# Kernel tuning notes

Measured on AMD Instinct MI355X. Metric: run time of the kernel, lower is better.

The kernel has to match this reference:

```python
import jax, jax.numpy as jnp
import numpy as np

NUM_LANDMARKS = 256
PINV_ITERS = 6


def iterative_inv(K):
    # Newton-Schulz iterative pseudo-inverse (Nystromformer), K: [B, m, m]
    I = jnp.eye(K.shape[-1], dtype=K.dtype)
    V = K.swapaxes(-1, -2) / (jnp.max(jnp.sum(K, axis=-2)) * jnp.max(jnp.sum(K, axis=-1)))
    for _ in range(PINV_ITERS):
        KV = K @ V
        V = 0.25 * V @ (13.0 * I - KV @ (15.0 * I - KV @ (7.0 * I - KV)))
    return V


def nystrom_attention_matrix(q, k, m):
    # q, k: [B, N, d] -> approximate softmax(q k^T / sqrt(d)) of shape [B, N, N]
    B, N, d = q.shape
    scale = 1.0 / jnp.sqrt(jnp.asarray(d, q.dtype))
    L = N // m
    q_l = q.reshape(B, m, L, d).mean(axis=2)  # landmark queries [B, m, d]
    k_l = k.reshape(B, m, L, d).mean(axis=2)  # landmark keys    [B, m, d]
    k1 = jax.nn.softmax(jnp.einsum('bnd,bmd->bnm', q, k_l) * scale, axis=-1)   # [B, N, m]
    k2 = jax.nn.softmax(jnp.einsum('bld,bmd->blm', q_l, k_l) * scale, axis=-1) # [B, m, m]
    k3 = jax.nn.softmax(jnp.einsum('bmd,bnd->bmn', q_l, k) * scale, axis=-1)   # [B, m, N]
    return (k1 @ iterative_inv(k2)) @ k3  # [B, N, N]


def setup_inputs() -> dict:
    key = jax.random.key(0)
    ks = jax.random.split(key, 8)
    B, C, T, W, H = 2, 64, 4, 32, 32
    d = C // 8
    scale = 0.05  # keep q.k scores in a sane softmax range
    return {
        'x': jax.random.normal(ks[0], (B, C, T, W, H), dtype=jnp.float32),
        'wq': jax.random.normal(ks[1], (d, C), dtype=jnp.float32) * scale,
        'bq': jax.random.normal(ks[2], (d,), dtype=jnp.float32) * scale,
        'wk': jax.random.normal(ks[3], (d, C), dtype=jnp.float32) * scale,
        'bk': jax.random.normal(ks[4], (d,), dtype=jnp.float32) * scale,
        'wv': jax.random.normal(ks[5], (C, C), dtype=jnp.float32) * scale,
        'bv': jax.random.normal(ks[6], (C,), dtype=jnp.float32) * scale,
        'gamma': jax.random.normal(ks[7], (1,), dtype=jnp.float32),
    }


def reference(x, wq, bq, wk, bk, wv, bv, gamma):
    B, C, T, W, H = x.shape
    N = T * W * H
    xf = x.reshape(B, C, N)
    # 1x1x1 Conv3d == per-token linear over channels
    q = jnp.einsum('oc,bcn->bno', wq, xf) + bq            # [B, N, C//8]
    k = jnp.einsum('oc,bcn->bno', wk, xf) + bk            # [B, N, C//8]
    v = jnp.einsum('oc,bcn->bon', wv, xf) + bv[None, :, None]  # [B, C, N]
    attn = nystrom_attention_matrix(q, k, NUM_LANDMARKS)  # [B, N, N]
    # out = bmm(value, attn^T): out[b,c,i] = sum_j v[b,c,j] * attn[b,i,j]
    out = jnp.einsum('bcj,bij->bci', v, attn).reshape(B, C, T, W, H)
    out = gamma[0] * out + x
    return out, attn
```

## Files before the change

kernel.cpp:

```cpp
#include <hip/hip_runtime.h>
#include <hip/hip_bf16.h>
#include <math.h>

#define NB 2
#define NC 64
#define ND 8
#define NN 4096
#define NM 256
#define NL 16
#define SCALE 0.35355339059327373f

typedef __attribute__((ext_vector_type(4))) float f32x4;
typedef __attribute__((ext_vector_type(8))) short bf16x8;

__device__ inline ushort f2bf(float f) {
  __hip_bfloat16 h = __float2bfloat16(f);
  return *reinterpret_cast<ushort*>(&h);
}
__device__ inline float bf2f(ushort u) {
  return __uint_as_float(((unsigned int)u) << 16);
}

__device__ inline void gl_lds16(const void* g, void* l) {
  __builtin_amdgcn_global_load_lds(
      (const __attribute__((address_space(1))) unsigned int*)g,
      (__attribute__((address_space(3))) unsigned int*)l, 16, 0, 0);
}

__global__ __launch_bounds__(256) void qkv2_kernel(
    const float* __restrict__ x,
    const float* __restrict__ wq, const float* __restrict__ bq,
    const float* __restrict__ wk, const float* __restrict__ bk,
    const float* __restrict__ wv, const float* __restrict__ bv,
    float* __restrict__ q, float* __restrict__ k, float* __restrict__ v) {
  __shared__ float ws[NC];
  int o = blockIdx.x;
  int b = blockIdx.z;
  int n0 = blockIdx.y * 1024;
  int t = threadIdx.x;
  const float* wrow;
  float bias;
  if (o < ND)            { wrow = wq + (size_t)o * NC;            bias = bq[o]; }
  else if (o < 2 * ND)   { wrow = wk + (size_t)(o - ND) * NC;     bias = bk[o - ND]; }
  else                   { wrow = wv + (size_t)(o - 2 * ND) * NC; bias = bv[o - 2 * ND]; }
  if (t < NC) ws[t] = wrow[t];
  __syncthreads();
  int n = n0 + t * 4;
  float4 acc = {bias, bias, bias, bias};
  #pragma unroll
  for (int c = 0; c < NC; ++c) {
    float wc = ws[c];
    float4 xv = *(const float4*)(x + ((size_t)b * NC + c) * NN + n);
    acc.x += wc * xv.x; acc.y += wc * xv.y; acc.z += wc * xv.z; acc.w += wc * xv.w;
  }
  if (o < ND) {
    float* qp = q + ((size_t)b * NN + n) * ND + o;
    qp[0] = acc.x; qp[8] = acc.y; qp[16] = acc.z; qp[24] = acc.w;
  } else if (o < 2 * ND) {
    float* kp = k + ((size_t)b * NN + n) * ND + (o - ND);
    kp[0] = acc.x; kp[8] = acc.y; kp[16] = acc.z; kp[24] = acc.w;
  } else {
    *(float4*)(v + ((size_t)b * NC + (o - 2 * ND)) * NN + n) = acc;
  }
}

__global__ void landmark_kernel(const float* __restrict__ q, const float* __restrict__ k,
                                float* __restrict__ ql, float* __restrict__ kl) {
  int idx = blockIdx.x * 256 + threadIdx.x;
  int b = idx / (NM * ND), r = idx % (NM * ND), i = r / ND, o = r % ND;
  float sq = 0.f, sk = 0.f;
  for (int l = 0; l < NL; ++l) {
    size_t base = ((size_t)b * NN + i * NL + l) * ND + o;
    sq += q[base]; sk += k[base];
  }
  ql[idx] = sq * (1.0f / NL);
  kl[idx] = sk * (1.0f / NL);
}

__global__ __launch_bounds__(256) void scores_softmax_m_bf16(
    const float* __restrict__ Q, int R, const float* __restrict__ KL,
    ushort* __restrict__ out) {
  __shared__ float skl[NM][9];
  int b = blockIdx.y;
  int t = threadIdx.x;
  for (int i = t; i < NM * ND; i += 256) skl[i >> 3][i & 7] = KL[(size_t)b * NM * ND + i];
  __syncthreads();
  int wave = t >> 6, lane = t & 63;
  int r = blockIdx.x * 4 + wave;
  const float* qrow = Q + ((size_t)b * R + r) * ND;
  float qr[ND];
  #pragma unroll
  for (int dd = 0; dd < ND; ++dd) qr[dd] = qrow[dd];
  float sc[4];
  float lmax = -1e30f;
  #pragma unroll
  for (int s = 0; s < 4; ++s) {
    int j = lane + 64 * s;
    float a = 0.f;
    #pragma unroll
    for (int dd = 0; dd < ND; ++dd) a += qr[dd] * skl[j][dd];
    sc[s] = a * SCALE;
    lmax = fmaxf(lmax, sc[s]);
  }
  for (int off = 32; off; off >>= 1) lmax = fmaxf(lmax, __shfl_xor(lmax, off));
  float lsum = 0.f;
  #pragma unroll
  for (int s = 0; s < 4; ++s) { sc[s] = expf(sc[s] - lmax); lsum += sc[s]; }
  for (int off = 32; off; off >>= 1) lsum += __shfl_xor(lsum, off);
  float inv = 1.0f / lsum;
  #pragma unroll
  for (int s = 0; s < 4; ++s)
    out[((size_t)b * R + r) * NM + lane + 64 * s] = f2bf(sc[s] * inv);
}

__global__ __launch_bounds__(256) void scores_softmax_m_f32(
    const float* __restrict__ Q, int R, const float* __restrict__ KL,
    float* __restrict__ out) {
  __shared__ float skl[NM][9];
  int b = blockIdx.y;
  int t = threadIdx.x;
  for (int i = t; i < NM * ND; i += 256) skl[i >> 3][i & 7] = KL[(size_t)b * NM * ND + i];
  __syncthreads();
  int wave = t >> 6, lane = t & 63;
  int r = blockIdx.x * 4 + wave;
  const float* qrow = Q + ((size_t)b * R + r) * ND;
  float qr[ND];
  #pragma unroll
  for (int dd = 0; dd < ND; ++dd) qr[dd] = qrow[dd];
  float sc[4];
  float lmax = -1e30f;
  #pragma unroll
  for (int s = 0; s < 4; ++s) {
    int j = lane + 64 * s;
    float a = 0.f;
    #pragma unroll
    for (int dd = 0; dd < ND; ++dd) a += qr[dd] * skl[j][dd];
    sc[s] = a * SCALE;
    lmax = fmaxf(lmax, sc[s]);
  }
  for (int off = 32; off; off >>= 1) lmax = fmaxf(lmax, __shfl_xor(lmax, off));
  float lsum = 0.f;
  #pragma unroll
  for (int s = 0; s < 4; ++s) { sc[s] = expf(sc[s] - lmax); lsum += sc[s]; }
  for (int off = 32; off; off >>= 1) lsum += __shfl_xor(lsum, off);
  float inv = 1.0f / lsum;
  #pragma unroll
  for (int s = 0; s < 4; ++s) out[((size_t)b * R + r) * NM + lane + 64 * s] = sc[s] * inv;
}

__global__ __launch_bounds__(256) void scores_softmax_n(
    const float* __restrict__ QL, const float* __restrict__ Kt,
    float* __restrict__ out) {
  __shared__ float wred[4], wsum[4];
  int b = blockIdx.y, i = blockIdx.x;
  int t = threadIdx.x;
  float qr[ND];
  #pragma unroll
  for (int dd = 0; dd < ND; ++dd) qr[dd] = QL[((size_t)b * NM + i) * ND + dd];
  float sc[16];
  float lmax = -1e30f;
  #pragma unroll
  for (int s = 0; s < 16; ++s) {
    int n = t + 256 * s;
    const float* kp = Kt + ((size_t)b * NN + n) * ND;
    float a = 0.f;
    #pragma unroll
    for (int dd = 0; dd < ND; ++dd) a += qr[dd] * kp[dd];
    sc[s] = a * SCALE;
    lmax = fmaxf(lmax, sc[s]);
  }
  for (int off = 32; off; off >>= 1) lmax = fmaxf(lmax, __shfl_xor(lmax, off));
  if ((t & 63) == 0) wred[t >> 6] = lmax;
  __syncthreads();
  lmax = fmaxf(fmaxf(wred[0], wred[1]), fmaxf(wred[2], wred[3]));
  float lsum = 0.f;
  #pragma unroll
  for (int s = 0; s < 16; ++s) { sc[s] = expf(sc[s] - lmax); lsum += sc[s]; }
  for (int off = 32; off; off >>= 1) lsum += __shfl_xor(lsum, off);
  if ((t & 63) == 0) wsum[t >> 6] = lsum;
  __syncthreads();
  lsum = wsum[0] + wsum[1] + wsum[2] + wsum[3];
  float inv = 1.0f / lsum;
  #pragma unroll
  for (int s = 0; s < 16; ++s) out[((size_t)b * NM + i) * NN + t + 256 * s] = sc[s] * inv;
}

__global__ __launch_bounds__(256) void denom_kernel(const float* __restrict__ k2,
                                                    float* __restrict__ denw) {
  __shared__ float red[256];
  int b = blockIdx.x;
  int t = threadIdx.x;
  float cs = 0.f;
  for (int i = 0; i < NM; ++i) cs += k2[((size_t)b * NM + i) * NM + t];
  red[t] = cs;
  __syncthreads();
  for (int off = 128; off; off >>= 1) {
    if (t < off) red[t] = fmaxf(red[t], red[t + off]);
    __syncthreads();
  }
  if (t == 0) denw[b] = red[0];
}

__global__ void vinit_kernel(const float* __restrict__ k2, const float* __restrict__ denw,
                             float* __restrict__ V) {
  int idx = blockIdx.x * 256 + threadIdx.x;
  int b = idx / (NM * NM), r = idx % (NM * NM), i = r / NM, j = r % NM;
  float dval = 1.0f / fmaxf(denw[0], denw[1]);
  V[idx] = k2[((size_t)b * NM + j) * NM + i] * dval;
}

__global__ __launch_bounds__(256) void gemm_rk32(
    const float* __restrict__ A, const float* __restrict__ Bm,
    float* __restrict__ out, float s_a, float s_ab) {
  int b = blockIdx.z;
  int bi = blockIdx.y * 32, bj = blockIdx.x * 32;
  __shared__ float As[32][260];
  __shared__ float Bs[256][36];
  int t = threadIdx.x;
  const float* Ab = A + (size_t)b * NM * NM;
  const float* Bb = Bm + (size_t)b * NM * NM;
  #pragma unroll
  for (int q = 0; q < 8; ++q) {
    int s = q * 256 + t;
    int ar = s >> 6, ac = (s & 63) * 4;
    *(float4*)&As[ar][ac] = *(const float4*)(Ab + (size_t)(bi + ar) * NM + ac);
    int br = s >> 3, bc = (s & 7) * 4;
    *(float4*)&Bs[br][bc] = *(const float4*)(Bb + (size_t)br * NM + bj + bc);
  }
  __syncthreads();
  int tx = t & 15, ty = t >> 4;
  float acc[2][2] = {};
  #pragma unroll 8
  for (int kk = 0; kk < NM; ++kk) {
    float a0 = As[ty * 2][kk], a1 = As[ty * 2 + 1][kk];
    float b0 = Bs[kk][tx * 2], b1 = Bs[kk][tx * 2 + 1];
    acc[0][0] += a0 * b0; acc[0][1] += a0 * b1;
    acc[1][0] += a1 * b0; acc[1][1] += a1 * b1;
  }
  #pragma unroll
  for (int i = 0; i < 2; ++i)
    #pragma unroll
    for (int j = 0; j < 2; ++j) {
      size_t o = ((size_t)b * NM + bi + ty * 2 + i) * NM + bj + tx * 2 + j;
      float r = s_ab * acc[i][j];
      if (s_a != 0.0f) r += s_a * A[o];
      out[o] = r;
    }
}

__global__ __launch_bounds__(256) void cvt_vinv_kernel(const float* __restrict__ Va,
                                                       ushort* __restrict__ Vt) {
  int b = blockIdx.z;
  int n0 = blockIdx.x * 32, m0 = blockIdx.y * 32;
  __shared__ float tile[32][33];
  int t = threadIdx.x;
  int r = t >> 3, c4 = (t & 7) * 4;
  float4 v = *(const float4*)(Va + ((size_t)b * NM + m0 + r) * NM + n0 + c4);
  tile[c4][r] = v.x; tile[c4 + 1][r] = v.y; tile[c4 + 2][r] = v.z; tile[c4 + 3][r] = v.w;
  __syncthreads();
  ushort4 u;
  u.x = f2bf(tile[r][c4]);     u.y = f2bf(tile[r][c4 + 1]);
  u.z = f2bf(tile[r][c4 + 2]); u.w = f2bf(tile[r][c4 + 3]);
  *(ushort4*)(Vt + ((size_t)b * NM + n0 + r) * NM + m0 + c4) = u;
}

__global__ __launch_bounds__(256) void cvt_t_kernel(const float* __restrict__ k3,
                                                    ushort* __restrict__ k3t) {
  int b = blockIdx.z;
  int n0 = blockIdx.x * 32, m0 = blockIdx.y * 32;
  __shared__ float tile[32][33];
  int t = threadIdx.x;
  int r = t >> 3, c4 = (t & 7) * 4;
  float4 v = *(const float4*)(k3 + ((size_t)b * NM + m0 + r) * NN + n0 + c4);
  tile[c4][r] = v.x; tile[c4 + 1][r] = v.y; tile[c4 + 2][r] = v.z; tile[c4 + 3][r] = v.w;
  __syncthreads();
  ushort4 u;
  u.x = f2bf(tile[r][c4]);     u.y = f2bf(tile[r][c4 + 1]);
  u.z = f2bf(tile[r][c4 + 2]); u.w = f2bf(tile[r][c4 + 3]);
  *(ushort4*)(k3t + ((size_t)b * NN + n0 + r) * NM + m0 + c4) = u;
}

__global__ __launch_bounds__(256) void gemm_a_mfma(
    const ushort* __restrict__ k1bf, const ushort* __restrict__ Vt,
    ushort* __restrict__ Abf) {
  int b = blockIdx.z;
  int bi = blockIdx.y * 128, bj = blockIdx.x * 128;
  __shared__ ushort As[128 * 64];
  __shared__ ushort Bs[128 * 64];
  int t = threadIdx.x;
  int wave = t >> 6, lane = t & 63;
  int wr = wave >> 1, wc = wave & 1;
  const ushort* Ab = k1bf + (size_t)b * NN * NM;
  const ushort* Bb = Vt + (size_t)b * NM * NM;
  f32x4 acc[4][4] = {};
  for (int k0 = 0; k0 < NM; k0 += 64) {
    #pragma unroll
    for (int q = 0; q < 4; ++q) {
      int s = q * 256 + t;
      int r = s >> 3, c = s & 7;
      int cs = (c ^ (r & 7)) << 3;
      gl_lds16(Ab + (size_t)(bi + r) * NM + k0 + cs, As + (size_t)s * 8);
      gl_lds16(Bb + (size_t)(bj + r) * NM + k0 + cs, Bs + (size_t)s * 8);
    }
    __syncthreads();
    #pragma unroll
    for (int kk = 0; kk < 2; ++kk) {
      int koff = kk * 64 + (lane >> 4) * 16;
      bf16x8 af[4], bfv[4];
      #pragma unroll
      for (int mi = 0; mi < 4; ++mi) {
        int row = wr * 64 + mi * 16 + (lane & 15);
        af[mi] = *(const bf16x8*)((const char*)As + row * 128 + (koff ^ ((row & 7) << 4)));
      }
      #pragma unroll
      for (int nj = 0; nj < 4; ++nj) {
        int row = wc * 64 + nj * 16 + (lane & 15);
        bfv[nj] = *(const bf16x8*)((const char*)Bs + row * 128 + (koff ^ ((row & 7) << 4)));
      }
      #pragma unroll
      for (int mi = 0; mi < 4; ++mi)
        #pragma unroll
        for (int nj = 0; nj < 4; ++nj)
          acc[mi][nj] = __builtin_amdgcn_mfma_f32_16x16x32_bf16(af[mi], bfv[nj], acc[mi][nj], 0, 0, 0);
    }
    __syncthreads();
  }
  int col = lane & 15, rbase = (lane >> 4) * 4;
  #pragma unroll
  for (int mi = 0; mi < 4; ++mi)
    #pragma unroll
    for (int nj = 0; nj < 4; ++nj)
      #pragma unroll
      for (int r = 0; r < 4; ++r)
        Abf[((size_t)b * NN + bi + wr * 64 + mi * 16 + rbase + r) * NM
            + bj + wc * 64 + nj * 16 + col] = f2bf(acc[mi][nj][r]);
}

__global__ __launch_bounds__(256) void gemm_attn_mfma(
    const ushort* __restrict__ Abf, const ushort* __restrict__ K3T,
    float* __restrict__ attn) {
  int lin = blockIdx.z * 1024 + blockIdx.y * 32 + blockIdx.x;
  int swz = (lin & 7) * 256 + (lin >> 3);
  int b = swz >> 10;
  int rem = swz & 1023;
  int bi = (rem >> 5) * 128, bj = (rem & 31) * 128;
  __shared__ ushort As[128 * 64];
  __shared__ ushort Bs[128 * 64];
  int t = threadIdx.x;
  int wave = t >> 6, lane = t & 63;
  int wr = wave >> 1, wc = wave & 1;
  const ushort* Ab = Abf + (size_t)b * NN * NM;
  const ushort* Bb = K3T + (size_t)b * NN * NM;
  f32x4 acc[4][4] = {};
  for (int k0 = 0; k0 < NM; k0 += 64) {
    #pragma unroll
    for (int q = 0; q < 4; ++q) {
      int s = q * 256 + t;
      int r = s >> 3, c = s & 7;
      int cs = (c ^ (r & 7)) << 3;
      gl_lds16(Ab + (size_t)(bi + r) * NM + k0 + cs, As + (size_t)s * 8);
      gl_lds16(Bb + (size_t)(bj + r) * NM + k0 + cs, Bs + (size_t)s * 8);
    }
    __syncthreads();
    #pragma unroll
    for (int kk = 0; kk < 2; ++kk) {
      int koff = kk * 64 + (lane >> 4) * 16;
      bf16x8 af[4], bfv[4];
      #pragma unroll
      for (int mi = 0; mi < 4; ++mi) {
        int row = wr * 64 + mi * 16 + (lane & 15);
        af[mi] = *(const bf16x8*)((const char*)As + row * 128 + (koff ^ ((row & 7) << 4)));
      }
      #pragma unroll
      for (int nj = 0; nj < 4; ++nj) {
        int row = wc * 64 + nj * 16 + (lane & 15);
        bfv[nj] = *(const bf16x8*)((const char*)Bs + row * 128 + (koff ^ ((row & 7) << 4)));
      }
      #pragma unroll
      for (int mi = 0; mi < 4; ++mi)
        #pragma unroll
        for (int nj = 0; nj < 4; ++nj)
          acc[mi][nj] = __builtin_amdgcn_mfma_f32_16x16x32_bf16(af[mi], bfv[nj], acc[mi][nj], 0, 0, 0);
    }
    __syncthreads();
  }
  int col = lane & 15, rbase = (lane >> 4) * 4;
  #pragma unroll
  for (int mi = 0; mi < 4; ++mi)
    #pragma unroll
    for (int nj = 0; nj < 4; ++nj)
      #pragma unroll
      for (int r = 0; r < 4; ++r)
        attn[((size_t)b * NN + bi + wr * 64 + mi * 16 + rbase + r) * NN
             + bj + wc * 64 + nj * 16 + col] = acc[mi][nj][r];
}

__global__ __launch_bounds__(256) void kv_kernel(
    const float* __restrict__ K3, const float* __restrict__ Vv,
    float* __restrict__ kvout) {
  int b = blockIdx.z, bp = blockIdx.x * 64;
  int j0base = blockIdx.y * (NN / 32);
  __shared__ float Ks[64][33], Vs[64][33];
  int t = threadIdx.x, tx = t & 15, ty = t >> 4;
  int lrow = t >> 2, ljc = (t & 3) * 8;
  float acc[4][4] = {};
  for (int j0 = j0base; j0 < j0base + NN / 32; j0 += 32) {
    float4 a0 = *(const float4*)(K3 + ((size_t)b * NM + bp + lrow) * NN + j0 + ljc);
    float4 a1 = *(const float4*)(K3 + ((size_t)b * NM + bp + lrow) * NN + j0 + ljc + 4);
    float4 v0 = *(const float4*)(Vv + ((size_t)b * NC + lrow) * NN + j0 + ljc);
    float4 v1 = *(const float4*)(Vv + ((size_t)b * NC + lrow) * NN + j0 + ljc + 4);
    Ks[lrow][ljc + 0] = a0.x; Ks[lrow][ljc + 1] = a0.y; Ks[lrow][ljc + 2] = a0.z; Ks[lrow][ljc + 3] = a0.w;
    Ks[lrow][ljc + 4] = a1.x; Ks[lrow][ljc + 5] = a1.y; Ks[lrow][ljc + 6] = a1.z; Ks[lrow][ljc + 7] = a1.w;
    Vs[lrow][ljc + 0] = v0.x; Vs[lrow][ljc + 1] = v0.y; Vs[lrow][ljc + 2] = v0.z; Vs[lrow][ljc + 3] = v0.w;
    Vs[lrow][ljc + 4] = v1.x; Vs[lrow][ljc + 5] = v1.y; Vs[lrow][ljc + 6] = v1.z; Vs[lrow][ljc + 7] = v1.w;
    __syncthreads();
    #pragma unroll
    for (int kk = 0; kk < 32; ++kk) {
      float av_[4], bv_[4];
      #pragma unroll
      for (int i = 0; i < 4; ++i) av_[i] = Ks[(ty << 2) + i][kk];
      #pragma unroll
      for (int j = 0; j < 4; ++j) bv_[j] = Vs[(tx << 2) + j][kk];
      #pragma unroll
      for (int i = 0; i < 4; ++i)
        #pragma unroll
        for (int j = 0; j < 4; ++j) acc[i][j] += av_[i] * bv_[j];
    }
    __syncthreads();
  }
  #pragma unroll
  for (int i = 0; i < 4; ++i)
    #pragma unroll
    for (int j = 0; j < 4; ++j)
      atomicAdd(&kvout[((size_t)b * NM + bp + (ty << 2) + i) * NC + (tx << 2) + j], acc[i][j]);
}

__global__ __launch_bounds__(256) void out_kernel(
    const ushort* __restrict__ Abf, const float* __restrict__ kvm,
    const float* __restrict__ x, const float* __restrict__ gamma,
    float* __restrict__ outp) {
  __shared__ float As[32 * 256];
  int blk = blockIdx.x;
  int b = blk / (NN / 32), n0 = (blk % (NN / 32)) * 32;
  int t = threadIdx.x;
  for (int it = 0; it < 32; ++it)
    As[it * 256 + (t ^ (it & 31))] = bf2f(Abf[((size_t)b * NN + n0 + it) * NM + t]);
  __syncthreads();
  int tn = t & 31, cg0 = (t >> 5) * 8;
  float g = gamma[0];
  float acc[8] = {};
  for (int p = 0; p < NM; ++p) {
    float a = As[tn * 256 + (p ^ (tn & 31))];
    float4 kv0 = *(const float4*)(kvm + ((size_t)b * NM + p) * NC + cg0);
    float4 kv1 = *(const float4*)(kvm + ((size_t)b * NM + p) * NC + cg0 + 4);
    acc[0] += a * kv0.x; acc[1] += a * kv0.y; acc[2] += a * kv0.z; acc[3] += a * kv0.w;
    acc[4] += a * kv1.x; acc[5] += a * kv1.y; acc[6] += a * kv1.z; acc[7] += a * kv1.w;
  }
  #pragma unroll
  for (int qd = 0; qd < 8; ++qd) {
    int c = cg0 + qd;
    size_t idx = ((size_t)b * NC + c) * NN + n0 + tn;
    outp[idx] = g * acc[qd] + x[idx];
  }
}

extern "C" void kernel_launch(void* const* d_in, const int* in_sizes, int n_in,
                              void* d_out, int out_size, void* d_ws, size_t ws_size,
                              hipStream_t stream) {
  const float* x     = (const float*)d_in[0];
  const float* wq    = (const float*)d_in[1];
  const float* bq    = (const float*)d_in[2];
  const float* wk    = (const float*)d_in[3];
  const float* bk    = (const float*)d_in[4];
  const float* wv    = (const float*)d_in[5];
  const float* bv    = (const float*)d_in[6];
  const float* gamma = (const float*)d_in[7];
  float* outp = (float*)d_out;
  float* attn = outp + (size_t)NB * NC * NN;
  float* w = (float*)d_ws;

  float* qw   = w;
  float* kw   = qw + 65536;
  float* vw   = kw + 65536;
  float* qlw  = vw + 524288;
  float* klw  = qlw + 4096;
  float* k1w  = klw + 4096;
  float* k2w  = k1w + 2097152;
  float* k3w  = k2w + 131072;
  float* Abuf = k3w + 2097152;
  float* Va   = Abuf + 2097152;
  float* Vb   = Va + 131072;
  float* Zb   = Vb + 131072;
  float* T1   = Zb + 131072;
  float* T2   = T1 + 131072;
  float* kvw  = T2 + 131072;
  float* denw = kvw + 32768;
  ushort* k1bf  = (ushort*)k1w;
  ushort* k3T   = (ushort*)k1w + 2097152;
  ushort* Abf   = (ushort*)Abuf;
  ushort* Vinvt = (ushort*)Zb;

  hipMemsetAsync(kvw, 0, (size_t)NB * NM * NC * sizeof(float), stream);
  qkv2_kernel<<<dim3(80, NN / 1024, NB), dim3(256), 0, stream>>>(
      x, wq, bq, wk, bk, wv, bv, qw, kw, vw);
  landmark_kernel<<<dim3(NB * NM * ND / 256), dim3(256), 0, stream>>>(qw, kw, qlw, klw);
  scores_softmax_m_bf16<<<dim3(NN / 4, NB), dim3(256), 0, stream>>>(qw, NN, klw, k1bf);
  scores_softmax_m_f32<<<dim3(NM / 4, NB), dim3(256), 0, stream>>>(qlw, NM, klw, k2w);
  scores_softmax_n<<<dim3(NM, NB), dim3(256), 0, stream>>>(qlw, kw, k3w);
  denom_kernel<<<dim3(NB), dim3(256), 0, stream>>>(k2w, denw);
  vinit_kernel<<<dim3(NB * NM * NM / 256), dim3(256), 0, stream>>>(k2w, denw, Va);

  float* Vc = Va; float* Vn = Vb;
  for (int it = 0; it < 6; ++it) {
    gemm_rk32<<<dim3(8, 8, NB), dim3(256), 0, stream>>>(k2w, Vc, Zb, 0.f, 1.f);
    gemm_rk32<<<dim3(8, 8, NB), dim3(256), 0, stream>>>(Zb, Zb, T1, 7.f, -1.f);
    gemm_rk32<<<dim3(8, 8, NB), dim3(256), 0, stream>>>(Zb, T1, T2, 15.f, -1.f);
    gemm_rk32<<<dim3(8, 8, NB), dim3(256), 0, stream>>>(Vc, T2, Vn, 3.25f, -0.25f);
    float* tmp = Vc; Vc = Vn; Vn = tmp;
  }

  cvt_vinv_kernel<<<dim3(NM / 32, NM / 32, NB), dim3(256), 0, stream>>>(Va, Vinvt);
  cvt_t_kernel<<<dim3(NN / 32, NM / 32, NB), dim3(256), 0, stream>>>(k3w, k3T);
  gemm_a_mfma<<<dim3(NM / 128, NN / 128, NB), dim3(256), 0, stream>>>(k1bf, Vinvt, Abf);
  gemm_attn_mfma<<<dim3(NN / 128, NN / 128, NB), dim3(256), 0, stream>>>(Abf, k3T, attn);
  kv_kernel<<<dim3(NM / 64, 32, NB), dim3(256), 0, stream>>>(k3w, vw, kvw);
  out_kernel<<<dim3(NB * NN / 32), dim3(256), 0, stream>>>(Abf, kvw, x, gamma, outp);
}
```

Before: 303.2 us.

## Fuse small kernels and split-K the Newton-Schulz GEMMs with lazy partial sums

The landmark mean is folded into the QKV projection through warp shuffles. The three softmax score kernels and the kv memset are merged into one multi-role launch, and the denominator is merged with the k3 transpose. Attention and kv GEMMs share one launch using a block swizzle. The Newton-Schulz GEMMs become split-K (two K halves written to separate buffers) with 64-thread blocks, and the consumer sums the partial buffers on load. V init is folded in via a transposed, scaled load mode. The aim is to cut launch count and raise parallelism in the small 256x256 iteration GEMMs, at the cost of extra partial-buffer traffic and low occupancy per block.

```diff
diff --git a/kernel.cpp b/kernel.cpp
--- a/kernel.cpp
+++ b/kernel.cpp
@@ -9,6 +9,7 @@
 #define NM 256
 #define NL 16
 #define SCALE 0.35355339059327373f
+#define PS (NB * NM * NM)
 
 typedef __attribute__((ext_vector_type(4))) float f32x4;
 typedef __attribute__((ext_vector_type(8))) short bf16x8;
@@ -27,12 +28,13 @@
       (__attribute__((address_space(3))) unsigned int*)l, 16, 0, 0);
 }
 
-__global__ __launch_bounds__(256) void qkv2_kernel(
+__global__ __launch_bounds__(256) void qkv2l_kernel(
     const float* __restrict__ x,
     const float* __restrict__ wq, const float* __restrict__ bq,
     const float* __restrict__ wk, const float* __restrict__ bk,
     const float* __restrict__ wv, const float* __restrict__ bv,
-    float* __restrict__ q, float* __restrict__ k, float* __restrict__ v) {
+    float* __restrict__ q, float* __restrict__ k, float* __restrict__ v,
+    float* __restrict__ ql, float* __restrict__ kl) {
   __shared__ float ws[NC];
   int o = blockIdx.x;
   int b = blockIdx.z;
@@ -62,222 +64,264 @@
   } else {
     *(float4*)(v + ((size_t)b * NC + (o - 2 * ND)) * NN + n) = acc;
   }
-}
-
-__global__ void landmark_kernel(const float* __restrict__ q, const float* __restrict__ k,
-                                float* __restrict__ ql, float* __restrict__ kl) {
-  int idx = blockIdx.x * 256 + threadIdx.x;
-  int b = idx / (NM * ND), r = idx % (NM * ND), i = r / ND, o = r % ND;
-  float sq = 0.f, sk = 0.f;
-  for (int l = 0; l < NL; ++l) {
-    size_t base = ((size_t)b * NN + i * NL + l) * ND + o;
-    sq += q[base]; sk += k[base];
-  }
-  ql[idx] = sq * (1.0f / NL);
-  kl[idx] = sk * (1.0f / NL);
-}
-
-__global__ __launch_bounds__(256) void scores_softmax_m_bf16(
-    const float* __restrict__ Q, int R, const float* __restrict__ KL,
-    ushort* __restrict__ out) {
+  if (o < 2 * ND) {
+    float s4 = acc.x + acc.y + acc.z + acc.w;
+    s4 += __shfl_xor(s4, 1);
+    s4 += __shfl_xor(s4, 2);
+    if ((t & 3) == 0) {
+      int g = n0 / 16 + (t >> 2);
+      float* dst = (o < ND) ? ql : kl;
+      dst[((size_t)b * NM + g) * ND + (o & 7)] = s4 * (1.0f / 16.0f);
+    }
+  }
+}
+
+__global__ __launch_bounds__(256) void scores_all_kernel(
+    const float* __restrict__ q, const float* __restrict__ ql,
+    const float* __restrict__ kw, const float* __restrict__ kl,
+    ushort* __restrict__ k1bf, float* __restrict__ k2w,
+    float* __restrict__ k3w, float* __restrict__ kvw) {
   __shared__ float skl[NM][9];
-  int b = blockIdx.y;
-  int t = threadIdx.x;
-  for (int i = t; i < NM * ND; i += 256) skl[i >> 3][i & 7] = KL[(size_t)b * NM * ND + i];
+  __shared__ float wred[4], wsum[4];
+  int blk = blockIdx.x;
+  int t = threadIdx.x;
+  if (blk < 2048 + 128) {
+    const float* Q; int R, b, xrow;
+    bool isbf;
+    if (blk < 2048) { b = blk >> 10; xrow = blk & 1023; Q = q;  R = NN; isbf = true; }
+    else { int r = blk - 2048; b = r >> 6; xrow = r & 63; Q = ql; R = NM; isbf = false; }
+    for (int i = t; i < NM * ND; i += 256) skl[i >> 3][i & 7] = kl[(size_t)b * NM * ND + i];
+    __syncthreads();
+    int wave = t >> 6, lane = t & 63;
+    int r = xrow * 4 + wave;
+    const float* qrow = Q + ((size_t)b * R + r) * ND;
+    float qr[ND];
+    #pragma unroll
+    for (int dd = 0; dd < ND; ++dd) qr[dd] = qrow[dd];
+    float sc[4];
+    float lmax = -1e30f;
+    #pragma unroll
+    for (int s = 0; s < 4; ++s) {
+      int j = lane + 64 * s;
+      float a = 0.f;
+      #pragma unroll
+      for (int dd = 0; dd < ND; ++dd) a += qr[dd] * skl[j][dd];
+      sc[s] = a * SCALE;
+      lmax = fmaxf(lmax, sc[s]);
+    }
+    for (int off = 32; off; off >>= 1) lmax = fmaxf(lmax, __shfl_xor(lmax, off));
+    float lsum = 0.f;
+    #pragma unroll
+    for (int s = 0; s < 4; ++s) { sc[s] = expf(sc[s] - lmax); lsum += sc[s]; }
+    for (int off = 32; off; off >>= 1) lsum += __shfl_xor(lsum, off);
+    float inv = 1.0f / lsum;
+    if (isbf) {
+      #pragma unroll
+      for (int s = 0; s < 4; ++s)
+        k1bf[((size_t)b * R + r) * NM + lane + 64 * s] = f2bf(sc[s] * inv);
+    } else {
+      #pragma unroll
+      for (int s = 0; s < 4; ++s)
+        k2w[((size_t)b * R + r) * NM + lane + 64 * s] = sc[s] * inv;
+    }
+  } else if (blk < 2048 + 128 + 512) {
+    int r = blk - 2176;
+    int b = r >> 8, i = r & 255;
+    float qr[ND];
+    #pragma unroll
+    for (int dd = 0; dd < ND; ++dd) qr[dd] = ql[((size_t)b * NM + i) * ND + dd];
+    float sc[16];
+    float lmax = -1e30f;
+    #pragma unroll
+    for (int s = 0; s < 16; ++s) {
+      int n = t + 256 * s;
+      const float* kp = kw + ((size_t)b * NN + n) * ND;
+      float a = 0.f;
+      #pragma unroll
+      for (int dd = 0; dd < ND; ++dd) a += qr[dd] * kp[dd];
+      sc[s] = a * SCALE;
+      lmax = fmaxf(lmax, sc[s]);
+    }
+    for (int off = 32; off; off >>= 1) lmax = fmaxf(lmax, __shfl_xor(lmax, off));
+    if ((t & 63) == 0) wred[t >> 6] = lmax;
+    __syncthreads();
+    lmax = fmaxf(fmaxf(wred[0], wred[1]), fmaxf(wred[2], wred[3]));
+    float lsum = 0.f;
+    #pragma unroll
+    for (int s = 0; s < 16; ++s) { sc[s] = expf(sc[s] - lmax); lsum += sc[s]; }
+    for (int off = 32; off; off >>= 1) lsum += __shfl_xor(lsum, off);
+    if ((t & 63) == 0) wsum[t >> 6] = lsum;
+    __syncthreads();
+    lsum = wsum[0] + wsum[1] + wsum[2] + wsum[3];
+    float inv = 1.0f / lsum;
+    #pragma unroll
+    for (int s = 0; s < 16; ++s) k3w[((size_t)b * NM + i) * NN + t + 256 * s] = sc[s] * inv;
+  } else {
+    int r = blk - 2688;
+    kvw[r * 256 + t] = 0.0f;
+  }
+}
+
+__global__ __launch_bounds__(256) void denom_k3t_kernel(
+    const float* __restrict__ k2, float* __restrict__ denw,
+    const float* __restrict__ k3, ushort* __restrict__ k3t) {
+  __shared__ float red[256];
+  __shared__ float tile[32][33];
+  int blk = blockIdx.x;
+  int t = threadIdx.x;
+  if (blk < NB) {
+    int b = blk;
+    float cs = 0.f;
+    for (int i = 0; i < NM; ++i) cs += k2[((size_t)b * NM + i) * NM + t];
+    red[t] = cs;
+    __syncthreads();
+    for (int off = 128; off; off >>= 1) {
+      if (t < off) red[t] = fmaxf(red[t], red[t + off]);
+      __syncthreads();
+    }
+    if (t == 0) denw[b] = red[0];
+  } else {
+    int r = blk - NB;
+    int n0 = (r & 127) * 32, m0 = ((r >> 7) & 7) * 32, b = r >> 10;
+    int rr = t >> 3, c4 = (t & 7) * 4;
+    float4 v = *(const float4*)(k3 + ((size_t)b * NM + m0 + rr) * NN + n0 + c4);
+    tile[c4][rr] = v.x; tile[c4 + 1][rr] = v.y; tile[c4 + 2][rr] = v.z; tile[c4 + 3][rr] = v.w;
+    __syncthreads();
+    ushort4 u;
+    u.x = f2bf(tile[rr][c4]);     u.y = f2bf(tile[rr][c4 + 1]);
+    u.z = f2bf(tile[rr][c4 + 2]); u.w = f2bf(tile[rr][c4 + 3]);
+    *(ushort4*)(k3t + ((size_t)b * NN + n0 + rr) * NM + m0 + c4) = u;
+  }
+}
+
+__global__ __launch_bounds__(64) void ns_gemm(
+    const float* __restrict__ A, int amode,
+    const float* __restrict__ B, int bmode,
+    const float* __restrict__ denw, float* __restrict__ O,
+    float s_a, float s_ab) {
+  __shared__ float As[128][36];
+  __shared__ float Bs[128][36];
+  int t = threadIdx.x;
+  int bj = blockIdx.x * 32, bi = blockIdx.y * 32;
+  int b = blockIdx.z >> 1, slice = blockIdx.z & 1;
+  int k0 = slice * 128;
+  size_t bo = (size_t)b * NM * NM;
+  float dval = (amode == 2 || bmode == 2) ? 1.0f / fmaxf(denw[0], denw[1]) : 0.f;
+  {
+    int r = t >> 1, kc0 = (t & 1) * 64;
+    if (amode == 2) {
+      for (int i = 0; i < 64; ++i) {
+        int kk = kc0 + i;
+        As[kk][r] = A[bo + (size_t)(k0 + kk) * NM + bi + r] * dval;
+      }
+    } else if (amode == 1) {
+      for (int i = 0; i < 16; ++i) {
+        const float* p = A + bo + (size_t)(bi + r) * NM + k0 + kc0 + i * 4;
+        float4 v0 = *(const float4*)p;
+        float4 v1 = *(const float4*)(p + PS);
+        As[kc0 + i * 4 + 0][r] = v0.x + v1.x;
+        As[kc0 + i * 4 + 1][r] = v0.y + v1.y;
+        As[kc0 + i * 4 + 2][r] = v0.z + v1.z;
+        As[kc0 + i * 4 + 3][r] = v0.w + v1.w;
+      }
+    } else {
+      for (int i = 0; i < 16; ++i) {
+        float4 v0 = *(const float4*)(A + bo + (size_t)(bi + r) * NM + k0 + kc0 + i * 4);
+        As[kc0 + i * 4 + 0][r] = v0.x;
+        As[kc0 + i * 4 + 1][r] = v0.y;
+        As[kc0 + i * 4 + 2][r] = v0.z;
+        As[kc0 + i * 4 + 3][r] = v0.w;
+      }
+    }
+    if (bmode == 2) {
+      for (int i2 = 0; i2 < 2; ++i2) {
+        int kr = t + 64 * i2;
+        for (int c = 0; c < 32; ++c)
+          Bs[kr][c] = B[bo + (size_t)(bj + c) * NM + k0 + kr] * dval;
+      }
+    } else if (bmode == 1) {
+      for (int i2 = 0; i2 < 2; ++i2) {
+        int kr = t + 64 * i2;
+        for (int c4 = 0; c4 < 32; c4 += 4) {
+          const float* p = B + bo + (size_t)(k0 + kr) * NM + bj + c4;
+          float4 v0 = *(const float4*)p;
+          float4 v1 = *(const float4*)(p + PS);
+          v0.x += v1.x; v0.y += v1.y; v0.z += v1.z; v0.w += v1.w;
+          *(float4*)&Bs[kr][c4] = v0;
+        }
+      }
+    } else {
+      for (int i2 = 0; i2 < 2; ++i2) {
+        int kr = t + 64 * i2;
+        for (int c4 = 0; c4 < 32; c4 += 4)
+          *(float4*)&Bs[kr][c4] =
+              *(const float4*)(B + bo + (size_t)(k0 + kr) * NM + bj + c4);
+      }
+    }
+  }
   __syncthreads();
-  int wave = t >> 6, lane = t & 63;
-  int r = blockIdx.x * 4 + wave;
-  const float* qrow = Q + ((size_t)b * R + r) * ND;
-  float qr[ND];
+  int tx = t & 7, ty = t >> 3;
+  float acc[4][4] = {};
+  #pragma unroll 4
+  for (int kk = 0; kk < 128; ++kk) {
+    float4 a4 = *(const float4*)&As[kk][ty * 4];
+    float4 b4 = *(const float4*)&Bs[kk][tx * 4];
+    float av[4] = {a4.x, a4.y, a4.z, a4.w};
+    float bv[4] = {b4.x, b4.y, b4.z, b4.w};
+    #pragma unroll
+    for (int i = 0; i < 4; ++i)
+      #pragma unroll
+      for (int j = 0; j < 4; ++j) acc[i][j] += av[i] * bv[j];
+  }
+  float* Op = O + (size_t)slice * PS + bo;
+  bool addA = (slice == 0) && (s_a != 0.0f);
   #pragma unroll
-  for (int dd = 0; dd < ND; ++dd) qr[dd] = qrow[dd];
-  float sc[4];
-  float lmax = -1e30f;
-  #pragma unroll
-  for (int s = 0; s < 4; ++s) {
-    int j = lane + 64 * s;
-    float a = 0.f;
-    #pragma unroll
-    for (int dd = 0; dd < ND; ++dd) a += qr[dd] * skl[j][dd];
-    sc[s] = a * SCALE;
-    lmax = fmaxf(lmax, sc[s]);
-  }
-  for (int off = 32; off; off >>= 1) lmax = fmaxf(lmax, __shfl_xor(lmax, off));
-  float lsum = 0.f;
-  #pragma unroll
-  for (int s = 0; s < 4; ++s) { sc[s] = expf(sc[s] - lmax); lsum += sc[s]; }
-  for (int off = 32; off; off >>= 1) lsum += __shfl_xor(lsum, off);
-  float inv = 1.0f / lsum;
-  #pragma unroll
-  for (int s = 0; s < 4; ++s)
-    out[((size_t)b * R + r) * NM + lane + 64 * s] = f2bf(sc[s] * inv);
-}
-
-__global__ __launch_bounds__(256) void scores_softmax_m_f32(
-    const float* __restrict__ Q, int R, const float* __restrict__ KL,
-    float* __restrict__ out) {
-  __shared__ float skl[NM][9];
-  int b = blockIdx.y;
-  int t = threadIdx.x;
-  for (int i = t; i < NM * ND; i += 256) skl[i >> 3][i & 7] = KL[(size_t)b * NM * ND + i];
-  __syncthreads();
-  int wave = t >> 6, lane = t & 63;
-  int r = blockIdx.x * 4 + wave;
-  const float* qrow = Q + ((size_t)b * R + r) * ND;
-  float qr[ND];
-  #pragma unroll
-  for (int dd = 0; dd < ND; ++dd) qr[dd] = qrow[dd];
-  float sc[4];
-  float lmax = -1e30f;
-  #pragma unroll
-  for (int s = 0; s < 4; ++s) {
-    int j = lane + 64 * s;
-    float a = 0.f;
-    #pragma unroll
-    for (int dd = 0; dd < ND; ++dd) a += qr[dd] * skl[j][dd];
-    sc[s] = a * SCALE;
-    lmax = fmaxf(lmax, sc[s]);
-  }
-  for (int off = 32; off; off >>= 1) lmax = fmaxf(lmax, __shfl_xor(lmax, off));
-  float lsum = 0.f;
-  #pragma unroll
-  for (int s = 0; s < 4; ++s) { sc[s] = expf(sc[s] - lmax); lsum += sc[s]; }
-  for (int off = 32; off; off >>= 1) lsum += __shfl_xor(lsum, off);
-  float inv = 1.0f / lsum;
-  #pragma unroll
-  for (int s = 0; s < 4; ++s) out[((size_t)b * R + r) * NM + lane + 64 * s] = sc[s] * inv;
-}
-
-__global__ __launch_bounds__(256) void scores_softmax_n(
-    const float* __restrict__ QL, const float* __restrict__ Kt,
-    float* __restrict__ out) {
-  __shared__ float wred[4], wsum[4];
-  int b = blockIdx.y, i = blockIdx.x;
-  int t = threadIdx.x;
-  float qr[ND];
-  #pragma unroll
-  for (int dd = 0; dd < ND; ++dd) qr[dd] = QL[((size_t)b * NM + i) * ND + dd];
-  float sc[16];
-  float lmax = -1e30f;
-  #pragma unroll
-  for (int s = 0; s < 16; ++s) {
-    int n = t + 256 * s;
-    const float* kp = Kt + ((size_t)b * NN + n) * ND;
-    float a = 0.f;
-    #pragma unroll
-    for (int dd = 0; dd < ND; ++dd) a += qr[dd] * kp[dd];
-    sc[s] = a * SCALE;
-    lmax = fmaxf(lmax, sc[s]);
-  }
-  for (int off = 32; off; off >>= 1) lmax = fmaxf(lmax, __shfl_xor(lmax, off));
-  if ((t & 63) == 0) wred[t >> 6] = lmax;
-  __syncthreads();
-  lmax = fmaxf(fmaxf(wred[0], wred[1]), fmaxf(wred[2], wred[3]));
-  float lsum = 0.f;
-  #pragma unroll
-  for (int s = 0; s < 16; ++s) { sc[s] = expf(sc[s] - lmax); lsum += sc[s]; }
-  for (int off = 32; off; off >>= 1) lsum += __shfl_xor(lsum, off);
-  if ((t & 63) == 0) wsum[t >> 6] = lsum;
-  __syncthreads();
-  lsum = wsum[0] + wsum[1] + wsum[2] + wsum[3];
-  float inv = 1.0f / lsum;
-  #pragma unroll
-  for (int s = 0; s < 16; ++s) out[((size_t)b * NM + i) * NN + t + 256 * s] = sc[s] * inv;
-}
-
-__global__ __launch_bounds__(256) void denom_kernel(const float* __restrict__ k2,
-                                                    float* __restrict__ denw) {
-  __shared__ float red[256];
-  int b = blockIdx.x;
-  int t = threadIdx.x;
-  float cs = 0.f;
-  for (int i = 0; i < NM; ++i) cs += k2[((size_t)b * NM + i) * NM + t];
-  red[t] = cs;
-  __syncthreads();
-  for (int off = 128; off; off >>= 1) {
-    if (t < off) red[t] = fmaxf(red[t], red[t + off]);
-    __syncthreads();
-  }
-  if (t == 0) denw[b] = red[0];
-}
-
-__global__ void vinit_kernel(const float* __restrict__ k2, const float* __restrict__ denw,
-                             float* __restrict__ V) {
-  int idx = blockIdx.x * 256 + threadIdx.x;
-  int b = idx / (NM * NM), r = idx % (NM * NM), i = r / NM, j = r % NM;
-  float dval = 1.0f / fmaxf(denw[0], denw[1]);
-  V[idx] = k2[((size_t)b * NM + j) * NM + i] * dval;
-}
-
-__global__ __launch_bounds__(256) void gemm_rk32(
-    const float* __restrict__ A, const float* __restrict__ Bm,
-    float* __restrict__ out, float s_a, float s_ab) {
-  int b = blockIdx.z;
-  int bi = blockIdx.y * 32, bj = blockIdx.x * 32;
-  __shared__ float As[32][260];
-  __shared__ float Bs[256][36];
-  int t = threadIdx.x;
-  const float* Ab = A + (size_t)b * NM * NM;
-  const float* Bb = Bm + (size_t)b * NM * NM;
-  #pragma unroll
-  for (int q = 0; q < 8; ++q) {
-    int s = q * 256 + t;
-    int ar = s >> 6, ac = (s & 63) * 4;
-    *(float4*)&As[ar][ac] = *(const float4*)(Ab + (size_t)(bi + ar) * NM + ac);
-    int br = s >> 3, bc = (s & 7) * 4;
-    *(float4*)&Bs[br][bc] = *(const float4*)(Bb + (size_t)br * NM + bj + bc);
-  }
-  __syncthreads();
-  int tx = t & 15, ty = t >> 4;
-  float acc[2][2] = {};
-  #pragma unroll 8
-  for (int kk = 0; kk < NM; ++kk) {
-    float a0 = As[ty * 2][kk], a1 = As[ty * 2 + 1][kk];
-    float b0 = Bs[kk][tx * 2], b1 = Bs[kk][tx * 2 + 1];
-    acc[0][0] += a0 * b0; acc[0][1] += a0 * b1;
-    acc[1][0] += a1 * b0; acc[1][1] += a1 * b1;
-  }
-  #pragma unroll
-  for (int i = 0; i < 2; ++i)
-    #pragma unroll
-    for (int j = 0; j < 2; ++j) {
-      size_t o = ((size_t)b * NM + bi + ty * 2 + i) * NM + bj + tx * 2 + j;
-      float r = s_ab * acc[i][j];
-      if (s_a != 0.0f) r += s_a * A[o];
-      out[o] = r;
-    }
-}
-
-__global__ __launch_bounds__(256) void cvt_vinv_kernel(const float* __restrict__ Va,
+  for (int i = 0; i < 4; ++i) {
+    int row = bi + ty * 4 + i;
+    float4 rv;
+    rv.x = s_ab * acc[i][0]; rv.y = s_ab * acc[i][1];
+    rv.z = s_ab * acc[i][2]; rv.w = s_ab * acc[i][3];
+    if (addA) {
+      int col = bj + tx * 4;
+      if (amode == 2) {
+        rv.x += s_a * A[bo + (size_t)(col + 0) * NM + row] * dval;
+        rv.y += s_a * A[bo + (size_t)(col + 1) * NM + row] * dval;
+        rv.z += s_a * A[bo + (size_t)(col + 2) * NM + row] * dval;
+        rv.w += s_a * A[bo + (size_t)(col + 3) * NM + row] * dval;
+      } else if (amode == 1) {
+        const float* p = A + bo + (size_t)row * NM + col;
+        float4 a0 = *(const float4*)p;
+        float4 a1 = *(const float4*)(p + PS);
+        rv.x += s_a * (a0.x + a1.x); rv.y += s_a * (a0.y + a1.y);
+        rv.z += s_a * (a0.z + a1.z); rv.w += s_a * (a0.w + a1.w);
+      } else {
+        float4 a0 = *(const float4*)(A + bo + (size_t)row * NM + col);
+        rv.x += s_a * a0.x; rv.y += s_a * a0.y;
+        rv.z += s_a * a0.z; rv.w += s_a * a0.w;
+      }
+    }
+    *(float4*)(Op + (size_t)row * NM + bj + tx * 4) = rv;
+  }
+}
+
+__global__ __launch_bounds__(256) void cvt_vinv_kernel(const float* __restrict__ Vp,
                                                        ushort* __restrict__ Vt) {
   int b = blockIdx.z;
   int n0 = blockIdx.x * 32, m0 = blockIdx.y * 32;
   __shared__ float tile[32][33];
   int t = threadIdx.x;
   int r = t >> 3, c4 = (t & 7) * 4;
-  float4 v = *(const float4*)(Va + ((size_t)b * NM + m0 + r) * NM + n0 + c4);
-  tile[c4][r] = v.x; tile[c4 + 1][r] = v.y; tile[c4 + 2][r] = v.z; tile[c4 + 3][r] = v.w;
+  size_t bo = (size_t)b * NM * NM;
+  const float* p = Vp + bo + (size_t)(m0 + r) * NM + n0 + c4;
+  float4 v0 = *(const float4*)p;
+  float4 v1 = *(const float4*)(p + PS);
+  tile[c4][r] = v0.x + v1.x; tile[c4 + 1][r] = v0.y + v1.y;
+  tile[c4 + 2][r] = v0.z + v1.z; tile[c4 + 3][r] = v0.w + v1.w;
   __syncthreads();
   ushort4 u;
   u.x = f2bf(tile[r][c4]);     u.y = f2bf(tile[r][c4 + 1]);
   u.z = f2bf(tile[r][c4 + 2]); u.w = f2bf(tile[r][c4 + 3]);
-  *(ushort4*)(Vt + ((size_t)b * NM + n0 + r) * NM + m0 + c4) = u;
-}
-
-__global__ __launch_bounds__(256) void cvt_t_kernel(const float* __restrict__ k3,
-                                                    ushort* __restrict__ k3t) {
-  int b = blockIdx.z;
-  int n0 = blockIdx.x * 32, m0 = blockIdx.y * 32;
-  __shared__ float tile[32][33];
-  int t = threadIdx.x;
-  int r = t >> 3, c4 = (t & 7) * 4;
-  float4 v = *(const float4*)(k3 + ((size_t)b * NM + m0 + r) * NN + n0 + c4);
-  tile[c4][r] = v.x; tile[c4 + 1][r] = v.y; tile[c4 + 2][r] = v.z; tile[c4 + 3][r] = v.w;
-  __syncthreads();
-  ushort4 u;
-  u.x = f2bf(tile[r][c4]);     u.y = f2bf(tile[r][c4 + 1]);
-  u.z = f2bf(tile[r][c4 + 2]); u.w = f2bf(tile[r][c4 + 3]);
-  *(ushort4*)(k3t + ((size_t)b * NN + n0 + r) * NM + m0 + c4) = u;
+  *(ushort4*)(Vt + bo + (size_t)(n0 + r) * NM + m0 + c4) = u;
 }
 
 __global__ __launch_bounds__(256) void gemm_a_mfma(
@@ -336,103 +380,108 @@
             + bj + wc * 64 + nj * 16 + col] = f2bf(acc[mi][nj][r]);
 }
 
-__global__ __launch_bounds__(256) void gemm_attn_mfma(
+__global__ __launch_bounds__(256) void attn_kv_kernel(
     const ushort* __restrict__ Abf, const ushort* __restrict__ K3T,
-    float* __restrict__ attn) {
-  int lin = blockIdx.z * 1024 + blockIdx.y * 32 + blockIdx.x;
-  int swz = (lin & 7) * 256 + (lin >> 3);
-  int b = swz >> 10;
-  int rem = swz & 1023;
-  int bi = (rem >> 5) * 128, bj = (rem & 31) * 128;
-  __shared__ ushort As[128 * 64];
-  __shared__ ushort Bs[128 * 64];
-  int t = threadIdx.x;
-  int wave = t >> 6, lane = t & 63;
-  int wr = wave >> 1, wc = wave & 1;
-  const ushort* Ab = Abf + (size_t)b * NN * NM;
-  const ushort* Bb = K3T + (size_t)b * NN * NM;
-  f32x4 acc[4][4] = {};
-  for (int k0 = 0; k0 < NM; k0 += 64) {
-    #pragma unroll
-    for (int q = 0; q < 4; ++q) {
-      int s = q * 256 + t;
-      int r = s >> 3, c = s & 7;
-      int cs = (c ^ (r & 7)) << 3;
-      gl_lds16(Ab + (size_t)(bi + r) * NM + k0 + cs, As + (size_t)s * 8);
-      gl_lds16(Bb + (size_t)(bj + r) * NM + k0 + cs, Bs + (size_t)s * 8);
-    }
-    __syncthreads();
-    #pragma unroll
-    for (int kk = 0; kk < 2; ++kk) {
-      int koff = kk * 64 + (lane >> 4) * 16;
-      bf16x8 af[4], bfv[4];
-      #pragma unroll
-      for (int mi = 0; mi < 4; ++mi) {
-        int row = wr * 64 + mi * 16 + (lane & 15);
-        af[mi] = *(const bf16x8*)((const char*)As + row * 128 + (koff ^ ((row & 7) << 4)));
-      }
-      #pragma unroll
-      for (int nj = 0; nj < 4; ++nj) {
-        int row = wc * 64 + nj * 16 + (lane & 15);
-        bfv[nj] = *(const bf16x8*)((const char*)Bs + row * 128 + (koff ^ ((row & 7) << 4)));
-      }
-      #pragma unroll
-      for (int mi = 0; mi < 4; ++mi)
-        #pragma unroll
-        for (int nj = 0; nj < 4; ++nj)
-          acc[mi][nj] = __builtin_amdgcn_mfma_f32_16x16x32_bf16(af[mi], bfv[nj], acc[mi][nj], 0, 0, 0);
-    }
-    __syncthreads();
-  }
-  int col = lane & 15, rbase = (lane >> 4) * 4;
-  #pragma unroll
-  for (int mi = 0; mi < 4; ++mi)
-    #pragma unroll
-    for (int nj = 0; nj < 4; ++nj)
-      #pragma unroll
-      for (int r = 0; r < 4; ++r)
-        attn[((size_t)b * NN + bi + wr * 64 + mi * 16 + rbase + r) * NN
-             + bj + wc * 64 + nj * 16 + col] = acc[mi][nj][r];
-}
-
-__global__ __launch_bounds__(256) void kv_kernel(
-    const float* __restrict__ K3, const float* __restrict__ Vv,
-    float* __restrict__ kvout) {
-  int b = blockIdx.z, bp = blockIdx.x * 64;
-  int j0base = blockIdx.y * (NN / 32);
-  __shared__ float Ks[64][33], Vs[64][33];
-  int t = threadIdx.x, tx = t & 15, ty = t >> 4;
-  int lrow = t >> 2, ljc = (t & 3) * 8;
-  float acc[4][4] = {};
-  for (int j0 = j0base; j0 < j0base + NN / 32; j0 += 32) {
-    float4 a0 = *(const float4*)(K3 + ((size_t)b * NM + bp + lrow) * NN + j0 + ljc);
-    float4 a1 = *(const float4*)(K3 + ((size_t)b * NM + bp + lrow) * NN + j0 + ljc + 4);
-    float4 v0 = *(const float4*)(Vv + ((size_t)b * NC + lrow) * NN + j0 + ljc);
-    float4 v1 = *(const float4*)(Vv + ((size_t)b * NC + lrow) * NN + j0 + ljc + 4);
-    Ks[lrow][ljc + 0] = a0.x; Ks[lrow][ljc + 1] = a0.y; Ks[lrow][ljc + 2] = a0.z; Ks[lrow][ljc + 3] = a0.w;
-    Ks[lrow][ljc + 4] = a1.x; Ks[lrow][ljc + 5] = a1.y; Ks[lrow][ljc + 6] = a1.z; Ks[lrow][ljc + 7] = a1.w;
-    Vs[lrow][ljc + 0] = v0.x; Vs[lrow][ljc + 1] = v0.y; Vs[lrow][ljc + 2] = v0.z; Vs[lrow][ljc + 3] = v0.w;
-    Vs[lrow][ljc + 4] = v1.x; Vs[lrow][ljc + 5] = v1.y; Vs[lrow][ljc + 6] = v1.z; Vs[lrow][ljc + 7] = v1.w;
-    __syncthreads();
-    #pragma unroll
-    for (int kk = 0; kk < 32; ++kk) {
-      float av_[4], bv_[4];
-      #pragma unroll
-      for (int i = 0; i < 4; ++i) av_[i] = Ks[(ty << 2) + i][kk];
-      #pragma unroll
-      for (int j = 0; j < 4; ++j) bv_[j] = Vs[(tx << 2) + j][kk];
-      #pragma unroll
-      for (int i = 0; i < 4; ++i)
-        #pragma unroll
-        for (int j = 0; j < 4; ++j) acc[i][j] += av_[i] * bv_[j];
-    }
-    __syncthreads();
-  }
-  #pragma unroll
-  for (int i = 0; i < 4; ++i)
-    #pragma unroll
-    for (int j = 0; j < 4; ++j)
-      atomicAdd(&kvout[((size_t)b * NM + bp + (ty << 2) + i) * NC + (tx << 2) + j], acc[i][j]);
+    float* __restrict__ attn, const float* __restrict__ k3w,
+    const float* __restrict__ vw, float* __restrict__ kvw) {
+  __shared__ char smem[32768];
+  int blk = blockIdx.x;
+  int t = threadIdx.x;
+  if (blk < 2048) {
+    ushort* As = (ushort*)smem;
+    ushort* Bs = (ushort*)(smem + 16384);
+    int swz = (blk & 7) * 256 + (blk >> 3);
+    int b = swz >> 10;
+    int rem = swz & 1023;
+    int bi = (rem >> 5) * 128, bj = (rem & 31) * 128;
+    int wave = t >> 6, lane = t & 63;
+    int wr = wave >> 1, wc = wave & 1;
+    const ushort* Ab = Abf + (size_t)b * NN * NM;
+    const ushort* Bb = K3T + (size_t)b * NN * NM;
+    f32x4 acc[4][4] = {};
+    for (int k0 = 0; k0 < NM; k0 += 64) {
+      #pragma unroll
+      for (int q = 0; q < 4; ++q) {
+        int s = q * 256 + t;
+        int r = s >> 3, c = s & 7;
+        int cs = (c ^ (r & 7)) << 3;
+        gl_lds16(Ab + (size_t)(bi + r) * NM + k0 + cs, As + (size_t)s * 8);
+        gl_lds16(Bb + (size_t)(bj + r) * NM + k0 + cs, Bs + (size_t)s * 8);
+      }
+      __syncthreads();
+      #pragma unroll
+      for (int kk = 0; kk < 2; ++kk) {
+        int koff = kk * 64 + (lane >> 4) * 16;
+        bf16x8 af[4], bfv[4];
+        #pragma unroll
+        for (int mi = 0; mi < 4; ++mi) {
+          int row = wr * 64 + mi * 16 + (lane & 15);
+          af[mi] = *(const bf16x8*)((const char*)As + row * 128 + (koff ^ ((row & 7) << 4)));
+        }
+        #pragma unroll
+        for (int nj = 0; nj < 4; ++nj) {
+          int row = wc * 64 + nj * 16 + (lane & 15);
+          bfv[nj] = *(const bf16x8*)((const char*)Bs + row * 128 + (koff ^ ((row & 7) << 4)));
+        }
+        #pragma unroll
+        for (int mi = 0; mi < 4; ++mi)
+          #pragma unroll
+          for (int nj = 0; nj < 4; ++nj)
+            acc[mi][nj] = __builtin_amdgcn_mfma_f32_16x16x32_bf16(af[mi], bfv[nj], acc[mi][nj], 0, 0, 0);
+      }
+      __syncthreads();
+    }
+    int col = lane & 15, rbase = (lane >> 4) * 4;
+    #pragma unroll
+    for (int mi = 0; mi < 4; ++mi)
+      #pragma unroll
+      for (int nj = 0; nj < 4; ++nj)
+        #pragma unroll
+        for (int r = 0; r < 4; ++r)
+          attn[((size_t)b * NN + bi + wr * 64 + mi * 16 + rbase + r) * NN
+               + bj + wc * 64 + nj * 16 + col] = acc[mi][nj][r];
+  } else {
+    typedef float KVRow[33];
+    KVRow* Ks = (KVRow*)smem;
+    KVRow* Vs = (KVRow*)(smem + 64 * 33 * 4);
+    int r = blk - 2048;
+    int bp = (r & 3) * 64;
+    int jsl = (r >> 2) & 31;
+    int b = r >> 7;
+    int j0base = jsl * (NN / 32);
+    int tx = t & 15, ty = t >> 4;
+    int lrow = t >> 2, ljc = (t & 3) * 8;
+    float acc[4][4] = {};
+    for (int j0 = j0base; j0 < j0base + NN / 32; j0 += 32) {
+      float4 a0 = *(const float4*)(k3w + ((size_t)b * NM + bp + lrow) * NN + j0 + ljc);
+      float4 a1 = *(const float4*)(k3w + ((size_t)b * NM + bp + lrow) * NN + j0 + ljc + 4);
+      float4 v0 = *(const float4*)(vw + ((size_t)b * NC + lrow) * NN + j0 + ljc);
+      float4 v1 = *(const float4*)(vw + ((size_t)b * NC + lrow) * NN + j0 + ljc + 4);
+      Ks[lrow][ljc + 0] = a0.x; Ks[lrow][ljc + 1] = a0.y; Ks[lrow][ljc + 2] = a0.z; Ks[lrow][ljc + 3] = a0.w;
+      Ks[lrow][ljc + 4] = a1.x; Ks[lrow][ljc + 5] = a1.y; Ks[lrow][ljc + 6] = a1.z; Ks[lrow][ljc + 7] = a1.w;
+      Vs[lrow][ljc + 0] = v0.x; Vs[lrow][ljc + 1] = v0.y; Vs[lrow][ljc + 2] = v0.z; Vs[lrow][ljc + 3] = v0.w;
+      Vs[lrow][ljc + 4] = v1.x; Vs[lrow][ljc + 5] = v1.y; Vs[lrow][ljc + 6] = v1.z; Vs[lrow][ljc + 7] = v1.w;
+      __syncthreads();
+      #pragma unroll
+      for (int kk = 0; kk < 32; ++kk) {
+        float av_[4], bv_[4];
+        #pragma unroll
+        for (int i = 0; i < 4; ++i) av_[i] = Ks[(ty << 2) + i][kk];
+        #pragma unroll
+        for (int j = 0; j < 4; ++j) bv_[j] = Vs[(tx << 2) + j][kk];
+        #pragma unroll
+        for (int i = 0; i < 4; ++i)
+          #pragma unroll
+          for (int j = 0; j < 4; ++j) acc[i][j] += av_[i] * bv_[j];
+      }
+      __syncthreads();
+    }
+    #pragma unroll
+    for (int i = 0; i < 4; ++i)
+      #pragma unroll
+      for (int j = 0; j < 4; ++j)
+        atomicAdd(&kvw[((size_t)b * NM + bp + (ty << 2) + i) * NC + (tx << 2) + j], acc[i][j]);
+  }
 }
 
 __global__ __launch_bounds__(256) void out_kernel(
@@ -488,41 +537,39 @@
   float* k2w  = k1w + 2097152;
   float* k3w  = k2w + 131072;
   float* Abuf = k3w + 2097152;
-  float* Va   = Abuf + 2097152;
-  float* Vb   = Va + 131072;
-  float* Zb   = Vb + 131072;
-  float* T1   = Zb + 131072;
-  float* T2   = T1 + 131072;
-  float* kvw  = T2 + 131072;
+  float* Zp   = Abuf + 1048576;
+  float* T1p  = Zp + 2 * PS;
+  float* T2p  = T1p + 2 * PS;
+  float* Vap  = T2p + 2 * PS;
+  float* Vbp  = Vap + 2 * PS;
+  float* kvw  = Vbp + 2 * PS;
   float* denw = kvw + 32768;
   ushort* k1bf  = (ushort*)k1w;
   ushort* k3T   = (ushort*)k1w + 2097152;
   ushort* Abf   = (ushort*)Abuf;
-  ushort* Vinvt = (ushort*)Zb;
-
-  hipMemsetAsync(kvw, 0, (size_t)NB * NM * NC * sizeof(float), stream);
-  qkv2_kernel<<<dim3(80, NN / 1024, NB), dim3(256), 0, stream>>>(
-      x, wq, bq, wk, bk, wv, bv, qw, kw, vw);
-  landmark_kernel<<<dim3(NB * NM * ND / 256), dim3(256), 0, stream>>>(qw, kw, qlw, klw);
-  scores_softmax_m_bf16<<<dim3(NN / 4, NB), dim3(256), 0, stream>>>(qw, NN, klw, k1bf);
-  scores_softmax_m_f32<<<dim3(NM / 4, NB), dim3(256), 0, stream>>>(qlw, NM, klw, k2w);
-  scores_softmax_n<<<dim3(NM, NB), dim3(256), 0, stream>>>(qlw, kw, k3w);
-  denom_kernel<<<dim3(NB), dim3(256), 0, stream>>>(k2w, denw);
-  vinit_kernel<<<dim3(NB * NM * NM / 256), dim3(256), 0, stream>>>(k2w, denw, Va);
-
-  float* Vc = Va; float* Vn = Vb;
+  ushort* Vinvt = (ushort*)Zp;
+
+  qkv2l_kernel<<<dim3(80, NN / 1024, NB), dim3(256), 0, stream>>>(
+      x, wq, bq, wk, bk, wv, bv, qw, kw, vw, qlw, klw);
+  scores_all_kernel<<<dim3(2048 + 128 + 512 + 128), dim3(256), 0, stream>>>(
+      qw, qlw, kw, klw, k1bf, k2w, k3w, kvw);
+  denom_k3t_kernel<<<dim3(NB + 2048), dim3(256), 0, stream>>>(k2w, denw, k3w, k3T);
+
+  const float* Vptr = k2w; int vmode = 2;
+  float* Vout = Vap;
+  float* Vfin = nullptr;
   for (int it = 0; it < 6; ++it) {
-    gemm_rk32<<<dim3(8, 8, NB), dim3(256), 0, stream>>>(k2w, Vc, Zb, 0.f, 1.f);
-    gemm_rk32<<<dim3(8, 8, NB), dim3(256), 0, stream>>>(Zb, Zb, T1, 7.f, -1.f);
-    gemm_rk32<<<dim3(8, 8, NB), dim3(256), 0, stream>>>(Zb, T1, T2, 15.f, -1.f);
-    gemm_rk32<<<dim3(8, 8, NB), dim3(256), 0, stream>>>(Vc, T2, Vn, 3.25f, -0.25f);
-    float* tmp = Vc; Vc = Vn; Vn = tmp;
-  }
-
-  cvt_vinv_kernel<<<dim3(NM / 32, NM / 32, NB), dim3(256), 0, stream>>>(Va, Vinvt);
-  cvt_t_kernel<<<dim3(NN / 32, NM / 32, NB), dim3(256), 0, stream>>>(k3w, k3T);
+    ns_gemm<<<dim3(8, 8, NB * 2), dim3(64), 0, stream>>>(k2w, 0, Vptr, vmode, denw, Zp, 0.f, 1.f);
+    ns_gemm<<<dim3(8, 8, NB * 2), dim3(64), 0, stream>>>(Zp, 1, Zp, 1, denw, T1p, 7.f, -1.f);
+    ns_gemm<<<dim3(8, 8, NB * 2), dim3(64), 0, stream>>>(Zp, 1, T1p, 1, denw, T2p, 15.f, -1.f);
+    ns_gemm<<<dim3(8, 8, NB * 2), dim3(64), 0, stream>>>(Vptr, vmode, T2p, 1, denw, Vout, 3.25f, -0.25f);
+    Vfin = Vout;
+    Vptr = Vout; vmode = 1;
+    Vout = (Vout == Vap) ? Vbp : Vap;
+  }
+
+  cvt_vinv_kernel<<<dim3(NM / 32, NM / 32, NB), dim3(256), 0, stream>>>(Vfin, Vinvt);
   gemm_a_mfma<<<dim3(NM / 128, NN / 128, NB), dim3(256), 0, stream>>>(k1bf, Vinvt, Abf);
-  gemm_attn_mfma<<<dim3(NN / 128, NN / 128, NB), dim3(256), 0, stream>>>(Abf, k3T, attn);
-  kv_kernel<<<dim3(NM / 64, 32, NB), dim3(256), 0, stream>>>(k3w, vw, kvw);
+  attn_kv_kernel<<<dim3(2048 + 256), dim3(256), 0, stream>>>(Abf, k3T, attn, k3w, vw, kvw);
   out_kernel<<<dim3(NB * NN / 32), dim3(256), 0, stream>>>(Abf, kvw, x, gamma, outp);
 }
```

New measurement: 328.8 us. 8.4% more time.
